# Optimization experiments

Hardware: AMD Instinct MI355X
Metric: run time of the kernel (lower is better)

The kernel has to match this reference:

```python
import jax, jax.numpy as jnp
import numpy as np

IN_FEATS = 602
N_HIDDEN = 256
N_CLASSES = 41
N_SRC0 = 292864   # block-1 src nodes (2-hop neighborhood)
N_DST0 = 11264    # block-1 dst == block-0 src (1-hop neighborhood)
N_DST1 = 1024     # seeds
FAN0 = 25         # neighbors per dst in block applied by layer 0
FAN1 = 10         # neighbors per dst in block applied by layer 1


def setup_inputs() -> dict:
    key = jax.random.key(0)
    ks = jax.random.split(key, 9)
    x = jax.random.normal(ks[0], (N_SRC0, IN_FEATS), dtype=jnp.float32)
    src_idx0 = jax.random.randint(ks[1], (N_DST0 * FAN0,), 0, N_SRC0)
    src_idx1 = jax.random.randint(ks[2], (N_DST1 * FAN1,), 0, N_DST0)
    s0 = 1.0 / np.sqrt(IN_FEATS)
    s1 = 1.0 / np.sqrt(N_HIDDEN)
    W_self0 = jax.random.uniform(ks[3], (IN_FEATS, N_HIDDEN), jnp.float32, -s0, s0)
    W_neigh0 = jax.random.uniform(ks[4], (IN_FEATS, N_HIDDEN), jnp.float32, -s0, s0)
    b0 = jnp.zeros((N_HIDDEN,), jnp.float32)
    W_self1 = jax.random.uniform(ks[5], (N_HIDDEN, N_CLASSES), jnp.float32, -s1, s1)
    W_neigh1 = jax.random.uniform(ks[6], (N_HIDDEN, N_CLASSES), jnp.float32, -s1, s1)
    b1 = jnp.zeros((N_CLASSES,), jnp.float32)
    return {"x": x, "W_self0": W_self0, "W_neigh0": W_neigh0, "b0": b0,
            "W_self1": W_self1, "W_neigh1": W_neigh1, "b1": b1,
            "src_idx0": src_idx0, "src_idx1": src_idx1}


def _sage_layer(h_src, h_dst, src_idx, fanout, W_self, W_neigh, b):
    # mean aggregation over exactly `fanout` sampled neighbors per dst node
    n_dst = h_dst.shape[0]
    h_neigh = h_src[src_idx].reshape(n_dst, fanout, -1).mean(axis=1)
    return h_dst @ W_self + h_neigh @ W_neigh + b


def reference(x, W_self0, W_neigh0, b0, W_self1, W_neigh1, b1, src_idx0, src_idx1):
    # layer 0: [N_SRC0, in] -> [N_DST0, hidden], relu; dropout is identity (eval mode)
    h = jax.nn.relu(_sage_layer(x, x[:N_DST0], src_idx0, FAN0, W_self0, W_neigh0, b0))
    # layer 1: [N_DST0, hidden] -> [N_DST1, classes], no activation
    out = _sage_layer(h, h[:N_DST1], src_idx1, FAN1, W_self1, W_neigh1, b1)
    return out
```

## Files before the change

kernel.cpp:

```cpp
#include <hip/hip_runtime.h>
#include <hip/hip_bf16.h>

#define IN_FEATS 602
#define N_HIDDEN 256
#define N_CLASSES 41
#define N_SRC0 292864
#define N_DST0 11264
#define N_DST1 1024
#define FAN0 25
#define FAN1 10
#define KPAD 1216
#define NAGG (N_DST0 / 4)
#define NWP ((KPAD / 32) * (N_HIDDEN / 32))

typedef __attribute__((ext_vector_type(4))) float f32x4;
typedef __attribute__((ext_vector_type(8))) short bf16x8;

static __device__ __forceinline__ unsigned pack_bf16x2(float lo, float hi) {
    unsigned a = __float_as_uint(lo);
    unsigned b = __float_as_uint(hi);
    a = (a + 0x7fffu + ((a >> 16) & 1u)) >> 16;
    b = (b + 0x7fffu + ((b >> 16) & 1u)) >> 16;
    return (a & 0xffffu) | (b << 16);
}

__global__ __launch_bounds__(256) void prep_kernel(
    const float* __restrict__ x,
    const int* __restrict__ idx,
    const float* __restrict__ Ws,
    const float* __restrict__ Wn,
    __hip_bfloat16* __restrict__ A,
    __hip_bfloat16* __restrict__ Wt)
{
    __shared__ __align__(16) char sm[32 * 33 * 4];

    if (blockIdx.x < NAGG) {
        int (*sidx)[FAN0] = (int(*)[FAN0])sm;
        const int wave = threadIdx.x >> 6;
        const int lane = threadIdx.x & 63;
        const int d = blockIdx.x * 4 + wave;

        if (lane < FAN0) sidx[wave][lane] = idx[d * FAN0 + lane];
        __syncthreads();

        unsigned* Arow = (unsigned*)(A + (size_t)d * KPAD);
        const float* xself = x + (size_t)d * IN_FEATS;

        if (lane < 6) Arow[602 + lane] = 0u;

        float accx[5], accy[5];
        #pragma unroll
        for (int c = 0; c < 5; ++c) { accx[c] = 0.f; accy[c] = 0.f; }

        #pragma unroll 5
        for (int n = 0; n < FAN0; ++n) {
            const float* xr = x + (size_t)sidx[wave][n] * IN_FEATS;
            #pragma unroll
            for (int c = 0; c < 5; ++c) {
                const int f = c * 128 + lane * 2;
                if (f < IN_FEATS) {
                    const float2 v = *(const float2*)&xr[f];
                    accx[c] += v.x; accy[c] += v.y;
                }
            }
        }

        #pragma unroll
        for (int c = 0; c < 5; ++c) {
            const int f = c * 128 + lane * 2;
            if (f < IN_FEATS) {
                const int f2 = f >> 1;
                const float2 sv = *(const float2*)&xself[f];
                Arow[f2] = pack_bf16x2(sv.x, sv.y);
                *(unsigned*)((char*)Arow + 1204 + f2 * 4) =
                    pack_bf16x2(accx[c] * (1.0f / FAN0), accy[c] * (1.0f / FAN0));
            }
        }
    } else {
        float (*tile)[33] = (float(*)[33])sm;
        const int b = blockIdx.x - NAGG;
        const int k0 = (b % (KPAD / 32)) * 32;
        const int n0 = (b / (KPAD / 32)) * 32;
        const int tx = threadIdx.x & 31, ty = threadIdx.x >> 5;

        #pragma unroll
        for (int i = 0; i < 4; ++i) {
            const int k = k0 + ty + i * 8;
            const int n = n0 + tx;
            float v = 0.f;
            if (k < IN_FEATS)            v = Ws[(size_t)k * N_HIDDEN + n];
            else if (k < 2 * IN_FEATS)   v = Wn[(size_t)(k - IN_FEATS) * N_HIDDEN + n];
            tile[ty + i * 8][tx] = v;
        }
        __syncthreads();
        #pragma unroll
        for (int i = 0; i < 4; ++i) {
            const int n = n0 + ty + i * 8;
            const int k = k0 + tx;
            Wt[(size_t)n * KPAD + k] = __float2bfloat16(tile[tx][ty + i * 8]);
        }
    }
}

#define BKK 64
#define LDSW 72

__global__ __launch_bounds__(256) void gemm0_mfma(
    const __hip_bfloat16* __restrict__ A,
    const __hip_bfloat16* __restrict__ Wt,
    const float* __restrict__ bias,
    float* __restrict__ h)
{
    __shared__ __hip_bfloat16 As[2][64 * LDSW];
    __shared__ __hip_bfloat16 Bs[2][64 * LDSW];

    const int D = blockIdx.x;
    const int s = D & 7;
    const int e = D >> 3;
    const int bx = e & 3;
    const int by = 8 * (e >> 2) + s;

    const int tid  = threadIdx.x;
    const int lane = tid & 63;
    const int wave = tid >> 6;
    const int wm = wave >> 1, wn = wave & 1;
    const int g = lane >> 4, r = lane & 15;
    const int m0 = by * 64, n0 = bx * 64;

    const int srow = tid >> 2;
    const int sc   = (tid & 3) * 16;
    const int sbase = srow * LDSW + sc;

    const size_t a_off = (size_t)(m0 + srow) * KPAD + sc;
    const size_t b_off = (size_t)(n0 + srow) * KPAD + sc;

    f32x4 acc[2][2] = {};

    float4 ra0, ra1, rb0, rb1;
    ra0 = *(const float4*)&A[a_off];      ra1 = *(const float4*)&A[a_off + 8];
    rb0 = *(const float4*)&Wt[b_off];     rb1 = *(const float4*)&Wt[b_off + 8];
    *(float4*)&As[0][sbase] = ra0;  *(float4*)&As[0][sbase + 8] = ra1;
    *(float4*)&Bs[0][sbase] = rb0;  *(float4*)&Bs[0][sbase + 8] = rb1;

    const int NT = KPAD / BKK;
    for (int t = 0; t < NT; ++t) {
        __syncthreads();
        const int cur = t & 1;

        if (t + 1 < NT) {
            const size_t k1 = (size_t)(t + 1) * BKK;
            ra0 = *(const float4*)&A[a_off + k1];      ra1 = *(const float4*)&A[a_off + k1 + 8];
            rb0 = *(const float4*)&Wt[b_off + k1];     rb1 = *(const float4*)&Wt[b_off + k1 + 8];
        }

        #pragma unroll
        for (int kh = 0; kh < 2; ++kh) {
            const bf16x8 af0 = *(const bf16x8*)&As[cur][(wm * 32 +      r) * LDSW + kh * 32 + g * 8];
            const bf16x8 af1 = *(const bf16x8*)&As[cur][(wm * 32 + 16 + r) * LDSW + kh * 32 + g * 8];
            const bf16x8 bf0 = *(const bf16x8*)&Bs[cur][(wn * 32 +      r) * LDSW + kh * 32 + g * 8];
            const bf16x8 bf1 = *(const bf16x8*)&Bs[cur][(wn * 32 + 16 + r) * LDSW + kh * 32 + g * 8];

            acc[0][0] = __builtin_amdgcn_mfma_f32_16x16x32_bf16(af0, bf0, acc[0][0], 0, 0, 0);
            acc[0][1] = __builtin_amdgcn_mfma_f32_16x16x32_bf16(af0, bf1, acc[0][1], 0, 0, 0);
            acc[1][0] = __builtin_amdgcn_mfma_f32_16x16x32_bf16(af1, bf0, acc[1][0], 0, 0, 0);
            acc[1][1] = __builtin_amdgcn_mfma_f32_16x16x32_bf16(af1, bf1, acc[1][1], 0, 0, 0);
        }

        if (t + 1 < NT) {
            const int nxt = cur ^ 1;
            *(float4*)&As[nxt][sbase] = ra0;  *(float4*)&As[nxt][sbase + 8] = ra1;
            *(float4*)&Bs[nxt][sbase] = rb0;  *(float4*)&Bs[nxt][sbase + 8] = rb1;
        }
    }

    #pragma unroll
    for (int mh = 0; mh < 2; ++mh)
        #pragma unroll
        for (int nh = 0; nh < 2; ++nh) {
            const int col = n0 + wn * 32 + nh * 16 + r;
            const float bv = bias[col];
            #pragma unroll
            for (int j = 0; j < 4; ++j) {
                const int row = m0 + wm * 32 + mh * 16 + g * 4 + j;
                const float v = acc[mh][nh][j] + bv;
                h[(size_t)row * N_HIDDEN + col] = fmaxf(v, 0.f);
            }
        }
}

__global__ __launch_bounds__(256) void tail_kernel(
    const float* __restrict__ h,
    const int* __restrict__ idx1,
    const float* __restrict__ Ws,
    const float* __restrict__ Wn,
    const float* __restrict__ b,
    float* __restrict__ out)
{
    const int w = threadIdx.x >> 6;
    const int lane = threadIdx.x & 63;
    const int d = blockIdx.x * 4 + w;

    __shared__ float hd[4][N_HIDDEN];
    __shared__ float hn[4][N_HIDDEN];
    __shared__ int sidx[4][FAN1];
    if (lane < FAN1) sidx[w][lane] = idx1[d * FAN1 + lane];
    __syncthreads();

    {
        const int k0 = lane * 4;
        const float4 self = *(const float4*)&h[(size_t)d * N_HIDDEN + k0];
        float ax = 0.f, ay = 0.f, az = 0.f, aw = 0.f;
        #pragma unroll
        for (int i = 0; i < FAN1; ++i) {
            const float4 v = *(const float4*)&h[(size_t)sidx[w][i] * N_HIDDEN + k0];
            ax += v.x; ay += v.y; az += v.z; aw += v.w;
        }
        *(float4*)&hd[w][k0] = self;
        hn[w][k0 + 0] = ax * (1.0f / FAN1);
        hn[w][k0 + 1] = ay * (1.0f / FAN1);
        hn[w][k0 + 2] = az * (1.0f / FAN1);
        hn[w][k0 + 3] = aw * (1.0f / FAN1);
    }
    __syncthreads();

    if (lane < N_CLASSES) {
        const int n = lane;
        float a0 = b[n], a1 = 0.f, a2 = 0.f, a3 = 0.f;
        #pragma unroll 4
        for (int k = 0; k < N_HIDDEN; k += 4) {
            a0 += hd[w][k + 0] * Ws[(k + 0) * N_CLASSES + n] + hn[w][k + 0] * Wn[(k + 0) * N_CLASSES + n];
            a1 += hd[w][k + 1] * Ws[(k + 1) * N_CLASSES + n] + hn[w][k + 1] * Wn[(k + 1) * N_CLASSES + n];
            a2 += hd[w][k + 2] * Ws[(k + 2) * N_CLASSES + n] + hn[w][k + 2] * Wn[(k + 2) * N_CLASSES + n];
            a3 += hd[w][k + 3] * Ws[(k + 3) * N_CLASSES + n] + hn[w][k + 3] * Wn[(k + 3) * N_CLASSES + n];
        }
        out[(size_t)d * N_CLASSES + n] = a0 + a1 + a2 + a3;
    }
}

extern "C" void kernel_launch(void* const* d_in, const int* in_sizes, int n_in,
                              void* d_out, int out_size, void* d_ws, size_t ws_size,
                              hipStream_t stream) {
    const float* x       = (const float*)d_in[0];
    const float* Wself0  = (const float*)d_in[1];
    const float* Wneigh0 = (const float*)d_in[2];
    const float* b0      = (const float*)d_in[3];
    const float* Wself1  = (const float*)d_in[4];
    const float* Wneigh1 = (const float*)d_in[5];
    const float* b1      = (const float*)d_in[6];
    const int*   idx0    = (const int*)d_in[7];
    const int*   idx1    = (const int*)d_in[8];
    float* out = (float*)d_out;

    __hip_bfloat16* Abf = (__hip_bfloat16*)d_ws;
    __hip_bfloat16* Wt  = Abf + (size_t)N_DST0 * KPAD;
    float*          h   = (float*)(Wt + (size_t)N_HIDDEN * KPAD);

    prep_kernel<<<NAGG + NWP, 256, 0, stream>>>(x, idx0, Wself0, Wneigh0, Abf, Wt);
    gemm0_mfma<<<(N_HIDDEN / 64) * (N_DST0 / 64), 256, 0, stream>>>(Abf, Wt, b0, h);
    tail_kernel<<<N_DST1 / 4, 256, 0, stream>>>(h, idx1, Wself1, Wneigh1, b1, out);
}
```

Measured before the change: 214.8 us.

## Sort neighbor indices and gather in address windows to improve cache locality

The aggregation part of the prep kernel now gives each wave up to three destination nodes instead of one and sorts each node's 25 neighbor indices with a rank sort in LDS. The gather then walks the source matrix in four address windows, with a block-wide barrier between windows, so that concurrently running waves touch similar regions of x and get more L2/MALL hits. Weight-transpose blocks are moved to the front of the grid, and launch bounds now request higher occupancy. In exchange it adds sorting work, extra barriers that can stall waves, and more accumulator registers per thread.

```diff
diff --git a/kernel.cpp b/kernel.cpp
--- a/kernel.cpp
+++ b/kernel.cpp
@@ -10,8 +10,11 @@
 #define FAN0 25
 #define FAN1 10
 #define KPAD 1216
-#define NAGG (N_DST0 / 4)
 #define NWP ((KPAD / 32) * (N_HIDDEN / 32))
+#define NAGGB 1024
+#define NWAVE (NAGGB * 4)
+#define NWIN 4
+#define WINSZ (N_SRC0 / NWIN)
 
 typedef __attribute__((ext_vector_type(4))) float f32x4;
 typedef __attribute__((ext_vector_type(8))) short bf16x8;
@@ -24,7 +27,7 @@
     return (a & 0xffffu) | (b << 16);
 }
 
-__global__ __launch_bounds__(256) void prep_kernel(
+__global__ __launch_bounds__(256, 4) void prep_kernel(
     const float* __restrict__ x,
     const int* __restrict__ idx,
     const float* __restrict__ Ws,
@@ -32,39 +35,103 @@
     __hip_bfloat16* __restrict__ A,
     __hip_bfloat16* __restrict__ Wt)
 {
-    __shared__ __align__(16) char sm[32 * 33 * 4];
-
-    if (blockIdx.x < NAGG) {
-        int (*sidx)[FAN0] = (int(*)[FAN0])sm;
-        const int wave = threadIdx.x >> 6;
-        const int lane = threadIdx.x & 63;
-        const int d = blockIdx.x * 4 + wave;
-
-        if (lane < FAN0) sidx[wave][lane] = idx[d * FAN0 + lane];
-        __syncthreads();
-
-        unsigned* Arow = (unsigned*)(A + (size_t)d * KPAD);
-        const float* xself = x + (size_t)d * IN_FEATS;
-
+    __shared__ __align__(16) char sm[4356];
+
+    if (blockIdx.x < NWP) {
+        float (*tile)[33] = (float(*)[33])sm;
+        const int b = blockIdx.x;
+        const int k0 = (b % (KPAD / 32)) * 32;
+        const int n0 = (b / (KPAD / 32)) * 32;
+        const int tx = threadIdx.x & 31, ty = threadIdx.x >> 5;
+
+        #pragma unroll
+        for (int i = 0; i < 4; ++i) {
+            const int k = k0 + ty + i * 8;
+            const int n = n0 + tx;
+            float v = 0.f;
+            if (k < IN_FEATS)            v = Ws[(size_t)k * N_HIDDEN + n];
+            else if (k < 2 * IN_FEATS)   v = Wn[(size_t)(k - IN_FEATS) * N_HIDDEN + n];
+            tile[ty + i * 8][tx] = v;
+        }
+        __syncthreads();
+        #pragma unroll
+        for (int i = 0; i < 4; ++i) {
+            const int n = n0 + ty + i * 8;
+            const int k = k0 + tx;
+            Wt[(size_t)n * KPAD + k] = __float2bfloat16(tile[tx][ty + i * 8]);
+        }
+        return;
+    }
+
+    const int b    = blockIdx.x - NWP;
+    const int wave = threadIdx.x >> 6;
+    const int lane = threadIdx.x & 63;
+    const int wid  = b * 4 + wave;
+    const int dcnt = (wid < N_DST0 - 2 * NWAVE) ? 3 : 2;
+    const int dstA[3] = { wid, wid + NWAVE, wid + 2 * NWAVE };
+
+    int (*srt)[3][FAN0] = (int(*)[3][FAN0])sm;
+    int (*raw)[FAN0]    = (int(*)[FAN0])(sm + 1216);
+
+    #pragma unroll
+    for (int d = 0; d < 3; ++d) {
+        if (d < dcnt && lane < FAN0)
+            raw[wave][lane] = idx[dstA[d] * FAN0 + lane];
+        __syncthreads();
+        if (d < dcnt && lane < FAN0) {
+            const int v = raw[wave][lane];
+            int rank = 0;
+            #pragma unroll
+            for (int j = 0; j < FAN0; ++j) {
+                const int u = raw[wave][j];
+                rank += (u < v) || (u == v && j < lane);
+            }
+            srt[wave][d][rank] = v;
+        }
+        __syncthreads();
+    }
+
+    float accx[3][5], accy[3][5];
+    #pragma unroll
+    for (int d = 0; d < 3; ++d)
+        #pragma unroll
+        for (int c = 0; c < 5; ++c) { accx[d][c] = 0.f; accy[d][c] = 0.f; }
+
+    int c0 = 0, c1 = 0, c2 = 0;
+
+#define GATHER_D(D, CUR) \
+    while (CUR < FAN0) { \
+        const int ri = srt[wave][D][CUR]; \
+        if (ri >= hi) break; \
+        const float* xr = x + (size_t)ri * IN_FEATS; \
+        _Pragma("unroll") \
+        for (int c = 0; c < 5; ++c) { \
+            const int f = c * 128 + lane * 2; \
+            if (f < IN_FEATS) { \
+                const float2 v = *(const float2*)&xr[f]; \
+                accx[D][c] += v.x; accy[D][c] += v.y; \
+            } \
+        } \
+        ++CUR; \
+    }
+
+    #pragma unroll 1
+    for (int w = 0; w < NWIN; ++w) {
+        const int hi = (w + 1) * WINSZ;
+        GATHER_D(0, c0)
+        GATHER_D(1, c1)
+        if (dcnt == 3) { GATHER_D(2, c2) }
+        __syncthreads();
+    }
+#undef GATHER_D
+
+    #pragma unroll
+    for (int d = 0; d < 3; ++d) {
+        if (d >= dcnt) break;
+        const int dd = dstA[d];
+        unsigned* Arow = (unsigned*)(A + (size_t)dd * KPAD);
+        const float* xself = x + (size_t)dd * IN_FEATS;
         if (lane < 6) Arow[602 + lane] = 0u;
-
-        float accx[5], accy[5];
-        #pragma unroll
-        for (int c = 0; c < 5; ++c) { accx[c] = 0.f; accy[c] = 0.f; }
-
-        #pragma unroll 5
-        for (int n = 0; n < FAN0; ++n) {
-            const float* xr = x + (size_t)sidx[wave][n] * IN_FEATS;
-            #pragma unroll
-            for (int c = 0; c < 5; ++c) {
-                const int f = c * 128 + lane * 2;
-                if (f < IN_FEATS) {
-                    const float2 v = *(const float2*)&xr[f];
-                    accx[c] += v.x; accy[c] += v.y;
-                }
-            }
-        }
-
         #pragma unroll
         for (int c = 0; c < 5; ++c) {
             const int f = c * 128 + lane * 2;
@@ -73,31 +140,8 @@
                 const float2 sv = *(const float2*)&xself[f];
                 Arow[f2] = pack_bf16x2(sv.x, sv.y);
                 *(unsigned*)((char*)Arow + 1204 + f2 * 4) =
-                    pack_bf16x2(accx[c] * (1.0f / FAN0), accy[c] * (1.0f / FAN0));
+                    pack_bf16x2(accx[d][c] * (1.0f / FAN0), accy[d][c] * (1.0f / FAN0));
             }
-        }
-    } else {
-        float (*tile)[33] = (float(*)[33])sm;
-        const int b = blockIdx.x - NAGG;
-        const int k0 = (b % (KPAD / 32)) * 32;
-        const int n0 = (b / (KPAD / 32)) * 32;
-        const int tx = threadIdx.x & 31, ty = threadIdx.x >> 5;
-
-        #pragma unroll
-        for (int i = 0; i < 4; ++i) {
-            const int k = k0 + ty + i * 8;
-            const int n = n0 + tx;
-            float v = 0.f;
-            if (k < IN_FEATS)            v = Ws[(size_t)k * N_HIDDEN + n];
-            else if (k < 2 * IN_FEATS)   v = Wn[(size_t)(k - IN_FEATS) * N_HIDDEN + n];
-            tile[ty + i * 8][tx] = v;
-        }
-        __syncthreads();
-        #pragma unroll
-        for (int i = 0; i < 4; ++i) {
-            const int n = n0 + ty + i * 8;
-            const int k = k0 + tx;
-            Wt[(size_t)n * KPAD + k] = __float2bfloat16(tile[tx][ty + i * 8]);
         }
     }
 }
@@ -255,7 +299,7 @@
     __hip_bfloat16* Wt  = Abf + (size_t)N_DST0 * KPAD;
     float*          h   = (float*)(Wt + (size_t)N_HIDDEN * KPAD);
 
-    prep_kernel<<<NAGG + NWP, 256, 0, stream>>>(x, idx0, Wself0, Wneigh0, Abf, Wt);
+    prep_kernel<<<NWP + NAGGB, 256, 0, stream>>>(x, idx0, Wself0, Wneigh0, Abf, Wt);
     gemm0_mfma<<<(N_HIDDEN / 64) * (N_DST0 / 64), 256, 0, stream>>>(Abf, Wt, b0, h);
     tail_kernel<<<N_DST1 / 4, 256, 0, stream>>>(h, idx1, Wself1, Wneigh1, b1, out);
 }
```

Measured after the change: 215.6 us. Within noise of the previous version (+0.4%).
